# Kernel optimization log

Hardware: AMD Instinct MI355X
Metric: run time of the kernel (lower is better)

## Reference

```python
import jax, jax.numpy as jnp
import numpy as np

E, N, D, H = 500000, 100000, 128, 128
LN_EPS = 1e-5


def setup_inputs() -> dict:
    key = jax.random.key(0)
    ks = jax.random.split(key, 8)
    efeat = jax.random.normal(ks[0], (E, D), dtype=jnp.float32)
    nfeat = jax.random.normal(ks[1], (N, D), dtype=jnp.float32)
    src = jax.random.randint(ks[2], (E,), 0, N, dtype=jnp.int64)
    dst = jax.random.randint(ks[3], (E,), 0, N, dtype=jnp.int64)
    dim_cat = 2 * D + D  # 2*input_dim_nodes + input_dim_edges = 384
    w1 = jax.random.normal(ks[4], (dim_cat, H), dtype=jnp.float32) / np.sqrt(dim_cat)
    b1 = jnp.zeros((H,), dtype=jnp.float32)
    w2 = jax.random.normal(ks[5], (H, D), dtype=jnp.float32) / np.sqrt(H)
    b2 = jnp.zeros((D,), dtype=jnp.float32)
    gamma = jnp.ones((D,), dtype=jnp.float32)
    beta = jnp.zeros((D,), dtype=jnp.float32)
    return {"efeat": efeat, "nfeat": nfeat, "src": src, "dst": dst,
            "w1": w1, "b1": b1, "w2": w2, "b2": b2, "gamma": gamma, "beta": beta}


def reference(efeat, nfeat, src, dst, w1, b1, w2, b2, gamma, beta):
    # gather per-edge src/dst node features and concat with edge features: [E, 2D+D]
    cat_feat = jnp.concatenate([efeat, nfeat[src], nfeat[dst]], axis=-1)
    # MeshGraphMLP with hidden_layers=1: Linear -> SiLU -> Linear -> LayerNorm
    h = jax.nn.silu(cat_feat @ w1 + b1)          # [E, H]
    y = h @ w2 + b2                               # [E, D]
    mu = jnp.mean(y, axis=-1, keepdims=True)
    var = jnp.mean((y - mu) ** 2, axis=-1, keepdims=True)
    y = (y - mu) * jax.lax.rsqrt(var + LN_EPS) * gamma + beta
    efeat_new = y + efeat                         # residual add
    return (efeat_new, nfeat)
```

## Files before the change

kernel.cpp:

```cpp
#include <hip/hip_runtime.h>

#define E_CONST 500000
#define N_CONST 100000

typedef __attribute__((ext_vector_type(8))) short bf16x8;
typedef __attribute__((ext_vector_type(4))) float f32x4;
typedef __attribute__((ext_vector_type(4))) unsigned u32x4;

__global__ __launch_bounds__(256) void prep_weights(const float* __restrict__ w1,
                                                    const float* __restrict__ w2,
                                                    short* __restrict__ ws) {
    int idx  = blockIdx.x * 256 + threadIdx.x;
    int frag = idx >> 9;
    int r    = idx & 511;
    int lane = r >> 3, j = r & 7;
    const float* w;
    int fi;
    if (frag < 96) { w = w1; fi = frag; }
    else           { w = w2; fi = frag - 96; }
    int kk = fi >> 3, nn = fi & 7;
    int k = kk * 32 + (lane >> 4) * 8 + j;
    int n = nn * 16 + (lane & 15);
    unsigned u = __float_as_uint(w[k * 128 + n]);
    u = u + 0x7FFFu + ((u >> 16) & 1u);
    ws[idx] = (short)(u >> 16);
}

__global__ __launch_bounds__(256) void copy_nfeat(const float* __restrict__ nfeat,
                                                  float* __restrict__ out) {
    size_t idx = (size_t)(blockIdx.x * 256 + threadIdx.x) * 4;
    *(f32x4*)(out + idx) = *(const f32x4*)(nfeat + idx);
}

__device__ __forceinline__ unsigned pack_bf16_trunc(float lo, float hi) {
    return __builtin_amdgcn_perm(__float_as_uint(hi), __float_as_uint(lo), 0x07060302u);
}

__device__ __forceinline__ bf16x8 pack8(f32x4 f0, f32x4 f1) {
    u32x4 pk;
    pk.x = pack_bf16_trunc(f0.x, f0.y);
    pk.y = pack_bf16_trunc(f0.z, f0.w);
    pk.z = pack_bf16_trunc(f1.x, f1.y);
    pk.w = pack_bf16_trunc(f1.z, f1.w);
    return __builtin_bit_cast(bf16x8, pk);
}

__global__ __launch_bounds__(256, 2) void edge_mlp(
    const float* __restrict__ efeat, const float* __restrict__ nfeat,
    const int* __restrict__ src, const int* __restrict__ dst,
    const short* __restrict__ wsw,
    const float* __restrict__ b1, const float* __restrict__ b2,
    const float* __restrict__ gamma, const float* __restrict__ beta,
    float* __restrict__ out) {

    __shared__ short As[64 * 264];
    __shared__ short hs[64 * 136];
    __shared__ float psum_s[256];
    __shared__ float psq_s[256];
    __shared__ float mu_s[64];
    __shared__ float rs_s[64];

    const int tid   = threadIdx.x;
    const int lane  = tid & 63;
    const int nw    = tid >> 6;
    const int l15   = lane & 15;
    const int quad  = lane >> 4;
    const int eBase = blockIdx.x * 64;

    bf16x8 b1f[2][12];
    bf16x8 b2f[2][4];
#pragma unroll
    for (int t = 0; t < 2; ++t) {
        int nn = nw * 2 + t;
#pragma unroll
        for (int kk = 0; kk < 12; ++kk)
            b1f[t][kk] = *(const bf16x8*)(wsw + ((kk * 8 + nn) * 64 + lane) * 8);
#pragma unroll
        for (int kk = 0; kk < 4; ++kk)
            b2f[t][kk] = *(const bf16x8*)(wsw + 49152 + ((kk * 8 + nn) * 64 + lane) * 8);
    }
    const float bb1[2] = { b1[nw * 32 + l15], b1[nw * 32 + 16 + l15] };
    const float bb2[2] = { b2[nw * 32 + l15], b2[nw * 32 + 16 + l15] };
    const float gg[2]  = { gamma[nw * 32 + l15], gamma[nw * 32 + 16 + l15] };
    const float bt[2]  = { beta[nw * 32 + l15],  beta[nw * 32 + 16 + l15] };

    {
        int r  = tid >> 1;
        int hf = tid & 1;
        int e  = eBase + (r & 63);
        if (e >= E_CONST) e = E_CONST - 1;
        int idx = (r < 64) ? src[e] : dst[e];
        const float* p = nfeat + (size_t)idx * 128 + hf * 64;
        short* wp = As + (r & 63) * 264 + (r >> 6) * 128 + hf * 64;
#pragma unroll 4
        for (int j = 0; j < 8; ++j) {
            f32x4 f0 = *(const f32x4*)(p + j * 8);
            f32x4 f1 = *(const f32x4*)(p + j * 8 + 4);
            *(bf16x8*)(wp + j * 8) = pack8(f0, f1);
        }
    }
    __syncthreads();

#pragma unroll 1
    for (int mt = 0; mt < 4; ++mt) {
        int e = eBase + mt * 16 + l15;
        if (e >= E_CONST) e = E_CONST - 1;
        const float* pe = efeat + (size_t)e * 128 + quad * 8;
        const short* ap = As + (mt * 16 + l15) * 264 + quad * 8;

        f32x4 acc0 = {0.f, 0.f, 0.f, 0.f}, acc1 = {0.f, 0.f, 0.f, 0.f};
#pragma unroll
        for (int kk = 0; kk < 4; ++kk) {
            f32x4 f0 = *(const f32x4*)(pe + kk * 32);
            f32x4 f1 = *(const f32x4*)(pe + kk * 32 + 4);
            bf16x8 a = pack8(f0, f1);
            acc0 = __builtin_amdgcn_mfma_f32_16x16x32_bf16(a, b1f[0][kk], acc0, 0, 0, 0);
            acc1 = __builtin_amdgcn_mfma_f32_16x16x32_bf16(a, b1f[1][kk], acc1, 0, 0, 0);
        }
#pragma unroll
        for (int kk = 4; kk < 12; ++kk) {
            bf16x8 a = *(const bf16x8*)(ap + (kk - 4) * 32);
            acc0 = __builtin_amdgcn_mfma_f32_16x16x32_bf16(a, b1f[0][kk], acc0, 0, 0, 0);
            acc1 = __builtin_amdgcn_mfma_f32_16x16x32_bf16(a, b1f[1][kk], acc1, 0, 0, 0);
        }
#pragma unroll
        for (int t = 0; t < 2; ++t) {
            f32x4 acc = (t == 0) ? acc0 : acc1;
            int col = nw * 32 + t * 16 + l15;
#pragma unroll
            for (int i = 0; i < 4; ++i) {
                float x  = acc[i] + bb1[t];
                float sg = __builtin_amdgcn_rcpf(1.0f + __expf(-x));
                float h  = x * sg;
                int row  = mt * 16 + quad * 4 + i;
                unsigned u = __float_as_uint(h);
                u = u + 0x7FFFu + ((u >> 16) & 1u);
                hs[row * 136 + col] = (short)(u >> 16);
            }
        }
    }
    __syncthreads();

    f32x4 y0[4], y1[4];
#pragma unroll
    for (int mt = 0; mt < 4; ++mt) {
        int arow = mt * 16 + l15;
        f32x4 acc0 = {0.f, 0.f, 0.f, 0.f}, acc1 = {0.f, 0.f, 0.f, 0.f};
#pragma unroll
        for (int kk = 0; kk < 4; ++kk) {
            bf16x8 a = *(const bf16x8*)(hs + arow * 136 + kk * 32 + quad * 8);
            acc0 = __builtin_amdgcn_mfma_f32_16x16x32_bf16(a, b2f[0][kk], acc0, 0, 0, 0);
            acc1 = __builtin_amdgcn_mfma_f32_16x16x32_bf16(a, b2f[1][kk], acc1, 0, 0, 0);
        }
        f32x4 bv0 = { bb2[0], bb2[0], bb2[0], bb2[0] };
        f32x4 bv1 = { bb2[1], bb2[1], bb2[1], bb2[1] };
        y0[mt] = acc0 + bv0;
        y1[mt] = acc1 + bv1;
    }

#pragma unroll
    for (int mt = 0; mt < 4; ++mt) {
#pragma unroll
        for (int i = 0; i < 4; ++i) {
            float a0 = y0[mt][i], a1 = y1[mt][i];
            float s = a0 + a1;
            float q = a0 * a0 + a1 * a1;
            s += __shfl_xor(s, 1);  q += __shfl_xor(q, 1);
            s += __shfl_xor(s, 2);  q += __shfl_xor(q, 2);
            s += __shfl_xor(s, 4);  q += __shfl_xor(q, 4);
            s += __shfl_xor(s, 8);  q += __shfl_xor(q, 8);
            if (l15 == 0) {
                int row = mt * 16 + quad * 4 + i;
                psum_s[row * 4 + nw] = s;
                psq_s [row * 4 + nw] = q;
            }
        }
    }
    __syncthreads();

    if (tid < 64) {
        f32x4 ps = *(const f32x4*)(psum_s + tid * 4);
        f32x4 pq = *(const f32x4*)(psq_s  + tid * 4);
        float mu = (ps.x + ps.y + ps.z + ps.w) * (1.0f / 128.0f);
        float m2 = (pq.x + pq.y + pq.z + pq.w) * (1.0f / 128.0f);
        mu_s[tid] = mu;
        rs_s[tid] = __builtin_amdgcn_rsqf(m2 - mu * mu + 1e-5f);
    }
    __syncthreads();

#pragma unroll
    for (int mt = 0; mt < 4; ++mt) {
#pragma unroll
        for (int i = 0; i < 4; ++i) {
            int row = mt * 16 + quad * 4 + i;
            int e = eBase + row;
            if (e < E_CONST) {
                float mu = mu_s[row], rs = rs_s[row];
                int col0 = nw * 32 + l15;
                const float* pef = efeat + (size_t)e * 128;
                float* po = out + (size_t)e * 128;
                po[col0]      = (y0[mt][i] - mu) * rs * gg[0] + bt[0] + pef[col0];
                po[col0 + 16] = (y1[mt][i] - mu) * rs * gg[1] + bt[1] + pef[col0 + 16];
            }
        }
    }
}

extern "C" void kernel_launch(void* const* d_in, const int* in_sizes, int n_in,
                              void* d_out, int out_size, void* d_ws, size_t ws_size,
                              hipStream_t stream) {
    const float* efeat = (const float*)d_in[0];
    const float* nfeat = (const float*)d_in[1];
    const int*   src   = (const int*)d_in[2];
    const int*   dst   = (const int*)d_in[3];
    const float* w1    = (const float*)d_in[4];
    const float* b1    = (const float*)d_in[5];
    const float* w2    = (const float*)d_in[6];
    const float* b2    = (const float*)d_in[7];
    const float* gamma = (const float*)d_in[8];
    const float* beta  = (const float*)d_in[9];
    float* out = (float*)d_out;
    short* wsw = (short*)d_ws;

    hipLaunchKernelGGL(prep_weights, dim3(256), dim3(256), 0, stream, w1, w2, wsw);
    hipLaunchKernelGGL(copy_nfeat, dim3(12500), dim3(256), 0, stream,
                       nfeat, out + (size_t)E_CONST * 128);
    hipLaunchKernelGGL(edge_mlp, dim3((E_CONST + 63) / 64), dim3(256), 0, stream,
                       efeat, nfeat, src, dst, wsw, b1, b2, gamma, beta, out);
}
```

Measured before the change: 749.1 us.

## Make edge MLP persistent with software-pipelined gather prefetch

Replaces the one-block-per-64-edges launch with a persistent grid of 1536 blocks, each looping over 32-edge tiles. Weight fragments are loaded into registers once per block rather than once per tile. The src/dst indices and node-feature gathers for later tiles are prefetched into registers two and three iterations ahead, so their latency overlaps the MFMA work. The hidden buffer is double-buffered and the LayerNorm reduction is folded to drop barriers, at the cost of more register pressure and a more complex schedule.

Result: slower. 1.046 ms (+39.7%).

```diff
diff --git a/kernel.cpp b/kernel.cpp
--- a/kernel.cpp
+++ b/kernel.cpp
@@ -2,9 +2,12 @@
 
 #define E_CONST 500000
 #define N_CONST 100000
+#define NT_CONST 15625
+#define GRID_MLP 1536
 
 typedef __attribute__((ext_vector_type(8))) short bf16x8;
 typedef __attribute__((ext_vector_type(4))) float f32x4;
+typedef __attribute__((ext_vector_type(2))) unsigned u32x2;
 typedef __attribute__((ext_vector_type(4))) unsigned u32x4;
 
 __global__ __launch_bounds__(256) void prep_weights(const float* __restrict__ w1,
@@ -45,6 +48,11 @@
     return __builtin_bit_cast(bf16x8, pk);
 }
 
+__device__ __forceinline__ void bar_lds() {
+    asm volatile("s_waitcnt lgkmcnt(0)" ::: "memory");
+    __builtin_amdgcn_s_barrier();
+}
+
 __global__ __launch_bounds__(256, 2) void edge_mlp(
     const float* __restrict__ efeat, const float* __restrict__ nfeat,
     const int* __restrict__ src, const int* __restrict__ dst,
@@ -53,19 +61,20 @@
     const float* __restrict__ gamma, const float* __restrict__ beta,
     float* __restrict__ out) {
 
-    __shared__ short As[64 * 264];
-    __shared__ short hs[64 * 136];
-    __shared__ float psum_s[256];
-    __shared__ float psq_s[256];
-    __shared__ float mu_s[64];
-    __shared__ float rs_s[64];
+    __shared__ short As[32 * 264];
+    __shared__ short hs[2][32 * 136];
+    __shared__ float psum_s[32 * 4];
+    __shared__ float psq_s[32 * 4];
 
     const int tid   = threadIdx.x;
     const int lane  = tid & 63;
     const int nw    = tid >> 6;
     const int l15   = lane & 15;
     const int quad  = lane >> 4;
-    const int eBase = blockIdx.x * 64;
+    const int g     = tid >> 3;
+    const int s8    = tid & 7;
+    const int grow  = g >> 2;
+    const int gpart = g & 3;
 
     bf16x8 b1f[2][12];
     bf16x8 b2f[2][4];
@@ -84,125 +93,175 @@
     const float gg[2]  = { gamma[nw * 32 + l15], gamma[nw * 32 + 16 + l15] };
     const float bt[2]  = { beta[nw * 32 + l15],  beta[nw * 32 + 16 + l15] };
 
-    {
-        int r  = tid >> 1;
-        int hf = tid & 1;
-        int e  = eBase + (r & 63);
-        if (e >= E_CONST) e = E_CONST - 1;
-        int idx = (r < 64) ? src[e] : dst[e];
-        const float* p = nfeat + (size_t)idx * 128 + hf * 64;
-        short* wp = As + (r & 63) * 264 + (r >> 6) * 128 + hf * 64;
-#pragma unroll 4
-        for (int j = 0; j < 8; ++j) {
-            f32x4 f0 = *(const f32x4*)(p + j * 8);
-            f32x4 f1 = *(const f32x4*)(p + j * 8 + 4);
-            *(bf16x8*)(wp + j * 8) = pack8(f0, f1);
-        }
-    }
-    __syncthreads();
-
+    int   ni[8];
+    f32x4 pf[8];
+
+    int t0 = blockIdx.x;
+
+#pragma unroll
+    for (int i = 0; i < 8; ++i) {
+        int e = t0 * 32 + grow + 8 * (i & 3);
+        ni[i] = (i < 4) ? src[e] : dst[e];
+    }
+#pragma unroll
+    for (int i = 0; i < 8; ++i)
+        pf[i] = *(const f32x4*)(nfeat + (size_t)ni[i] * 128 + gpart * 32 + s8 * 4);
+#pragma unroll
+    for (int i = 0; i < 8; ++i) {
+        int row = grow + 8 * (i & 3) + ((i >> 2) << 5);
+        u32x2 w;
+        w.x = pack_bf16_trunc(pf[i].x, pf[i].y);
+        w.y = pack_bf16_trunc(pf[i].z, pf[i].w);
+        *(u32x2*)(As + (row & 31) * 264 + (row >> 5) * 128 + gpart * 32 + s8 * 4) = w;
+    }
+    if (t0 + GRID_MLP < NT_CONST) {
+#pragma unroll
+        for (int i = 0; i < 8; ++i) {
+            int e = (t0 + GRID_MLP) * 32 + grow + 8 * (i & 3);
+            ni[i] = (i < 4) ? src[e] : dst[e];
+        }
+    }
+    bar_lds();
+    if (t0 + GRID_MLP < NT_CONST) {
+#pragma unroll
+        for (int i = 0; i < 8; ++i)
+            pf[i] = *(const f32x4*)(nfeat + (size_t)ni[i] * 128 + gpart * 32 + s8 * 4);
+    }
+    if (t0 + 2 * GRID_MLP < NT_CONST) {
+#pragma unroll
+        for (int i = 0; i < 8; ++i) {
+            int e = (t0 + 2 * GRID_MLP) * 32 + grow + 8 * (i & 3);
+            ni[i] = (i < 4) ? src[e] : dst[e];
+        }
+    }
+
+    int cur = 0;
 #pragma unroll 1
-    for (int mt = 0; mt < 4; ++mt) {
-        int e = eBase + mt * 16 + l15;
-        if (e >= E_CONST) e = E_CONST - 1;
-        const float* pe = efeat + (size_t)e * 128 + quad * 8;
-        const short* ap = As + (mt * 16 + l15) * 264 + quad * 8;
-
-        f32x4 acc0 = {0.f, 0.f, 0.f, 0.f}, acc1 = {0.f, 0.f, 0.f, 0.f};
-#pragma unroll
-        for (int kk = 0; kk < 4; ++kk) {
-            f32x4 f0 = *(const f32x4*)(pe + kk * 32);
-            f32x4 f1 = *(const f32x4*)(pe + kk * 32 + 4);
-            bf16x8 a = pack8(f0, f1);
-            acc0 = __builtin_amdgcn_mfma_f32_16x16x32_bf16(a, b1f[0][kk], acc0, 0, 0, 0);
-            acc1 = __builtin_amdgcn_mfma_f32_16x16x32_bf16(a, b1f[1][kk], acc1, 0, 0, 0);
-        }
-#pragma unroll
-        for (int kk = 4; kk < 12; ++kk) {
-            bf16x8 a = *(const bf16x8*)(ap + (kk - 4) * 32);
-            acc0 = __builtin_amdgcn_mfma_f32_16x16x32_bf16(a, b1f[0][kk], acc0, 0, 0, 0);
-            acc1 = __builtin_amdgcn_mfma_f32_16x16x32_bf16(a, b1f[1][kk], acc1, 0, 0, 0);
-        }
-#pragma unroll
-        for (int t = 0; t < 2; ++t) {
-            f32x4 acc = (t == 0) ? acc0 : acc1;
-            int col = nw * 32 + t * 16 + l15;
+    for (int t = t0; t < NT_CONST; t += GRID_MLP) {
+        short* hb = &hs[cur][0];
+
+#pragma unroll
+        for (int mt = 0; mt < 2; ++mt) {
+            size_t e = (size_t)t * 32 + mt * 16 + l15;
+            const float* pe = efeat + e * 128 + quad * 8;
+            const short* ap = As + (mt * 16 + l15) * 264 + quad * 8;
+
+            f32x4 ef[8];
+#pragma unroll
+            for (int kk = 0; kk < 4; ++kk) {
+                ef[kk * 2]     = *(const f32x4*)(pe + kk * 32);
+                ef[kk * 2 + 1] = *(const f32x4*)(pe + kk * 32 + 4);
+            }
+            f32x4 acc0 = {0.f, 0.f, 0.f, 0.f}, acc1 = {0.f, 0.f, 0.f, 0.f};
+#pragma unroll
+            for (int kk = 4; kk < 12; ++kk) {
+                bf16x8 a = *(const bf16x8*)(ap + (kk - 4) * 32);
+                acc0 = __builtin_amdgcn_mfma_f32_16x16x32_bf16(a, b1f[0][kk], acc0, 0, 0, 0);
+                acc1 = __builtin_amdgcn_mfma_f32_16x16x32_bf16(a, b1f[1][kk], acc1, 0, 0, 0);
+            }
+#pragma unroll
+            for (int kk = 0; kk < 4; ++kk) {
+                bf16x8 a = pack8(ef[kk * 2], ef[kk * 2 + 1]);
+                acc0 = __builtin_amdgcn_mfma_f32_16x16x32_bf16(a, b1f[0][kk], acc0, 0, 0, 0);
+                acc1 = __builtin_amdgcn_mfma_f32_16x16x32_bf16(a, b1f[1][kk], acc1, 0, 0, 0);
+            }
+#pragma unroll
+            for (int tt = 0; tt < 2; ++tt) {
+                f32x4 acc = (tt == 0) ? acc0 : acc1;
+                int col = nw * 32 + tt * 16 + l15;
+#pragma unroll
+                for (int i = 0; i < 4; ++i) {
+                    float x  = acc[i] + bb1[tt];
+                    float sg = __builtin_amdgcn_rcpf(1.0f + __expf(-x));
+                    float h  = x * sg;
+                    int row  = mt * 16 + quad * 4 + i;
+                    unsigned u = __float_as_uint(h);
+                    u = u + 0x7FFFu + ((u >> 16) & 1u);
+                    hb[row * 136 + col] = (short)(u >> 16);
+                }
+            }
+        }
+        bar_lds();
+
+        if (t + GRID_MLP < NT_CONST) {
+#pragma unroll
+            for (int i = 0; i < 8; ++i) {
+                int row = grow + 8 * (i & 3) + ((i >> 2) << 5);
+                u32x2 w;
+                w.x = pack_bf16_trunc(pf[i].x, pf[i].y);
+                w.y = pack_bf16_trunc(pf[i].z, pf[i].w);
+                *(u32x2*)(As + (row & 31) * 264 + (row >> 5) * 128 + gpart * 32 + s8 * 4) = w;
+            }
+        }
+        if (t + 2 * GRID_MLP < NT_CONST) {
+#pragma unroll
+            for (int i = 0; i < 8; ++i)
+                pf[i] = *(const f32x4*)(nfeat + (size_t)ni[i] * 128 + gpart * 32 + s8 * 4);
+        }
+
+        f32x4 y0[2], y1[2];
+#pragma unroll
+        for (int mt = 0; mt < 2; ++mt) {
+            int arow = mt * 16 + l15;
+            f32x4 acc0 = {0.f, 0.f, 0.f, 0.f}, acc1 = {0.f, 0.f, 0.f, 0.f};
+#pragma unroll
+            for (int kk = 0; kk < 4; ++kk) {
+                bf16x8 a = *(const bf16x8*)(hb + arow * 136 + kk * 32 + quad * 8);
+                acc0 = __builtin_amdgcn_mfma_f32_16x16x32_bf16(a, b2f[0][kk], acc0, 0, 0, 0);
+                acc1 = __builtin_amdgcn_mfma_f32_16x16x32_bf16(a, b2f[1][kk], acc1, 0, 0, 0);
+            }
+            f32x4 bv0 = { bb2[0], bb2[0], bb2[0], bb2[0] };
+            f32x4 bv1 = { bb2[1], bb2[1], bb2[1], bb2[1] };
+            y0[mt] = acc0 + bv0;
+            y1[mt] = acc1 + bv1;
+        }
+
+#pragma unroll
+        for (int mt = 0; mt < 2; ++mt) {
 #pragma unroll
             for (int i = 0; i < 4; ++i) {
-                float x  = acc[i] + bb1[t];
-                float sg = __builtin_amdgcn_rcpf(1.0f + __expf(-x));
-                float h  = x * sg;
-                int row  = mt * 16 + quad * 4 + i;
-                unsigned u = __float_as_uint(h);
-                u = u + 0x7FFFu + ((u >> 16) & 1u);
-                hs[row * 136 + col] = (short)(u >> 16);
-            }
-        }
-    }
-    __syncthreads();
-
-    f32x4 y0[4], y1[4];
-#pragma unroll
-    for (int mt = 0; mt < 4; ++mt) {
-        int arow = mt * 16 + l15;
-        f32x4 acc0 = {0.f, 0.f, 0.f, 0.f}, acc1 = {0.f, 0.f, 0.f, 0.f};
-#pragma unroll
-        for (int kk = 0; kk < 4; ++kk) {
-            bf16x8 a = *(const bf16x8*)(hs + arow * 136 + kk * 32 + quad * 8);
-            acc0 = __builtin_amdgcn_mfma_f32_16x16x32_bf16(a, b2f[0][kk], acc0, 0, 0, 0);
-            acc1 = __builtin_amdgcn_mfma_f32_16x16x32_bf16(a, b2f[1][kk], acc1, 0, 0, 0);
-        }
-        f32x4 bv0 = { bb2[0], bb2[0], bb2[0], bb2[0] };
-        f32x4 bv1 = { bb2[1], bb2[1], bb2[1], bb2[1] };
-        y0[mt] = acc0 + bv0;
-        y1[mt] = acc1 + bv1;
-    }
-
-#pragma unroll
-    for (int mt = 0; mt < 4; ++mt) {
-#pragma unroll
-        for (int i = 0; i < 4; ++i) {
-            float a0 = y0[mt][i], a1 = y1[mt][i];
-            float s = a0 + a1;
-            float q = a0 * a0 + a1 * a1;
-            s += __shfl_xor(s, 1);  q += __shfl_xor(q, 1);
-            s += __shfl_xor(s, 2);  q += __shfl_xor(q, 2);
-            s += __shfl_xor(s, 4);  q += __shfl_xor(q, 4);
-            s += __shfl_xor(s, 8);  q += __shfl_xor(q, 8);
-            if (l15 == 0) {
+                float a0 = y0[mt][i], a1 = y1[mt][i];
+                float su = a0 + a1;
+                float q  = a0 * a0 + a1 * a1;
+                su += __shfl_xor(su, 1);  q += __shfl_xor(q, 1);
+                su += __shfl_xor(su, 2);  q += __shfl_xor(q, 2);
+                su += __shfl_xor(su, 4);  q += __shfl_xor(q, 4);
+                su += __shfl_xor(su, 8);  q += __shfl_xor(q, 8);
+                if (l15 == 0) {
+                    int row = mt * 16 + quad * 4 + i;
+                    psum_s[row * 4 + nw] = su;
+                    psq_s [row * 4 + nw] = q;
+                }
+            }
+        }
+        bar_lds();
+
+#pragma unroll
+        for (int mt = 0; mt < 2; ++mt) {
+#pragma unroll
+            for (int i = 0; i < 4; ++i) {
                 int row = mt * 16 + quad * 4 + i;
-                psum_s[row * 4 + nw] = s;
-                psq_s [row * 4 + nw] = q;
-            }
-        }
-    }
-    __syncthreads();
-
-    if (tid < 64) {
-        f32x4 ps = *(const f32x4*)(psum_s + tid * 4);
-        f32x4 pq = *(const f32x4*)(psq_s  + tid * 4);
-        float mu = (ps.x + ps.y + ps.z + ps.w) * (1.0f / 128.0f);
-        float m2 = (pq.x + pq.y + pq.z + pq.w) * (1.0f / 128.0f);
-        mu_s[tid] = mu;
-        rs_s[tid] = __builtin_amdgcn_rsqf(m2 - mu * mu + 1e-5f);
-    }
-    __syncthreads();
-
-#pragma unroll
-    for (int mt = 0; mt < 4; ++mt) {
-#pragma unroll
-        for (int i = 0; i < 4; ++i) {
-            int row = mt * 16 + quad * 4 + i;
-            int e = eBase + row;
-            if (e < E_CONST) {
-                float mu = mu_s[row], rs = rs_s[row];
+                f32x4 ps = *(const f32x4*)(psum_s + row * 4);
+                f32x4 pq = *(const f32x4*)(psq_s  + row * 4);
+                float mu = (ps.x + ps.y + ps.z + ps.w) * (1.0f / 128.0f);
+                float m2 = (pq.x + pq.y + pq.z + pq.w) * (1.0f / 128.0f);
+                float rs = __builtin_amdgcn_rsqf(m2 - mu * mu + 1e-5f);
+                size_t e = (size_t)t * 32 + row;
                 int col0 = nw * 32 + l15;
-                const float* pef = efeat + (size_t)e * 128;
-                float* po = out + (size_t)e * 128;
+                const float* pef = efeat + e * 128;
+                float* po = out + e * 128;
                 po[col0]      = (y0[mt][i] - mu) * rs * gg[0] + bt[0] + pef[col0];
                 po[col0 + 16] = (y1[mt][i] - mu) * rs * gg[1] + bt[1] + pef[col0 + 16];
             }
         }
+        if (t + 3 * GRID_MLP < NT_CONST) {
+#pragma unroll
+            for (int i = 0; i < 8; ++i) {
+                int e = (t + 3 * GRID_MLP) * 32 + grow + 8 * (i & 3);
+                ni[i] = (i < 4) ? src[e] : dst[e];
+            }
+        }
+        cur ^= 1;
     }
 }
 
@@ -225,6 +284,6 @@
     hipLaunchKernelGGL(prep_weights, dim3(256), dim3(256), 0, stream, w1, w2, wsw);
     hipLaunchKernelGGL(copy_nfeat, dim3(12500), dim3(256), 0, stream,
                        nfeat, out + (size_t)E_CONST * 128);
-    hipLaunchKernelGGL(edge_mlp, dim3((E_CONST + 63) / 64), dim3(256), 0, stream,
+    hipLaunchKernelGGL(edge_mlp, dim3(GRID_MLP), dim3(256), 0, stream,
                        efeat, nfeat, src, dst, wsw, b1, b2, gamma, beta, out);
 }
```
